# Kernel optimization log

Hardware: AMD Instinct MI355X
Metric: run time of the kernel (lower is better)

The kernel has to match this reference:

```python
import jax, jax.numpy as jnp
import numpy as np

N_HEAD = 16
N_KV_HEAD = 8
HEAD_DIM = 64
EPS_NORM = 1e-6


def _rms_norm(x):
    # F.rms_norm without learned weight
    return x * jax.lax.rsqrt(jnp.mean(x * x, axis=-1, keepdims=True) + EPS_NORM)


def _apply_rotary_emb(x, cos, sin):
    # x: [B, T, H, D]; cos/sin: [T, 1, D/2] (broadcast over B and H)
    d = x.shape[-1] // 2
    x1, x2 = x[..., :d], x[..., d:]
    return jnp.concatenate([x1 * cos + x2 * sin, -x1 * sin + x2 * cos], axis=-1)


def setup_inputs() -> dict:
    key = jax.random.key(0)
    ks = jax.random.split(key, 8)
    B, T, C = 2, 2048, 1024
    return {
        "x": jax.random.normal(ks[0], (B, T, C), jnp.float32),
        "cos": jax.random.uniform(ks[1], (T, 1, HEAD_DIM // 2), jnp.float32),
        "sin": jax.random.uniform(ks[2], (T, 1, HEAD_DIM // 2), jnp.float32),
        "Wq": jax.random.normal(ks[3], (N_HEAD * HEAD_DIM, C), jnp.float32) * 0.02,
        "Wk": jax.random.normal(ks[4], (N_KV_HEAD * HEAD_DIM, C), jnp.float32) * 0.02,
        "Wv": jax.random.normal(ks[5], (N_KV_HEAD * HEAD_DIM, C), jnp.float32) * 0.02,
        "Wproj": jax.random.normal(ks[6], (C, C), jnp.float32) * 0.02,
        "w_braid": jax.random.normal(ks[7], (HEAD_DIM,), jnp.float32),
    }


def reference(x, cos, sin, Wq, Wk, Wv, Wproj, w_braid):
    B, T, C = x.shape
    q = (x @ Wq.T).reshape(B, T, N_HEAD, HEAD_DIM)
    k = (x @ Wk.T).reshape(B, T, N_KV_HEAD, HEAD_DIM)
    v = (x @ Wv.T).reshape(B, T, N_KV_HEAD, HEAD_DIM)
    q = _rms_norm(_apply_rotary_emb(q, cos, sin))
    k = _rms_norm(_apply_rotary_emb(k, cos, sin))
    # [B, H, T, D]
    q = q.transpose(0, 2, 1, 3)
    k = k.transpose(0, 2, 1, 3)
    v = v.transpose(0, 2, 1, 3)
    rep = N_HEAD // N_KV_HEAD
    k = jnp.repeat(k, rep, axis=1)  # GQA repeat_kv_heads
    v = jnp.repeat(v, rep, axis=1)
    # rank-1 outer-sum score: s_q[i] + s_k[j]
    s_q = jnp.einsum("bhtd,d->bht", q, w_braid)
    s_k = jnp.einsum("bhsd,d->bhs", k, w_braid)
    scores = s_q[..., :, None] + s_k[..., None, :]  # [B, H, T, T]
    causal = jnp.arange(T)[:, None] >= jnp.arange(T)[None, :]
    scores = jnp.where(causal, scores, -jnp.inf)
    attn = jax.nn.sigmoid(scores)  # non-softmax gating
    y = jnp.einsum("bhts,bhsd->bhtd", attn, v)
    y = y / (T ** 0.5 + 1e-6)
    y = y.transpose(0, 2, 1, 3).reshape(B, T, C)
    return y @ Wproj.T
```

## Files before the change

kernel.cpp:

```cpp
#include <hip/hip_runtime.h>

#define BATCH   2
#define T_LEN   2048
#define C_DIM   1024
#define NH      16
#define NKV     8
#define HD      64

typedef unsigned short u16;
typedef __attribute__((ext_vector_type(8))) short short8;
typedef __attribute__((ext_vector_type(4))) float floatx4;

__device__ __forceinline__ u16 f2bf(float f) {
    union { float f; unsigned u; } v; v.f = f;
    unsigned r = v.u + 0x7FFF + ((v.u >> 16) & 1);
    return (u16)(r >> 16);
}

__device__ __forceinline__ float bf2f(u16 b) {
    union { unsigned u; float f; } v; v.u = ((unsigned)b) << 16;
    return v.f;
}

__device__ __forceinline__ void gload_lds16(const u16* g, u16* l) {
    __builtin_amdgcn_global_load_lds(
        (const __attribute__((address_space(1))) void*)g,
        (__attribute__((address_space(3))) void*)l, 16, 0, 0);
}

__global__ __launch_bounds__(256)
void cvt_all(const float* __restrict__ x, const float* __restrict__ Wq,
             const float* __restrict__ Wk, const float* __restrict__ Wv,
             const float* __restrict__ Wp, u16* __restrict__ xb,
             u16* __restrict__ Wqkvb, u16* __restrict__ Wpb) {
    const int blk = blockIdx.x;
    const float* src; u16* dst; long off;
    if (blk < 4096)      { src = x;  dst = xb;              off = (long)blk * 1024; }
    else if (blk < 5120) { src = Wq; dst = Wqkvb;           off = (long)(blk - 4096) * 1024; }
    else if (blk < 5632) { src = Wk; dst = Wqkvb + 1048576; off = (long)(blk - 5120) * 1024; }
    else if (blk < 6144) { src = Wv; dst = Wqkvb + 1572864; off = (long)(blk - 5632) * 1024; }
    else                 { src = Wp; dst = Wpb;             off = (long)(blk - 6144) * 1024; }
    const long i = off + (long)threadIdx.x * 4;
    const float4 f = *(const float4*)&src[i];
    ushort4 o;
    o.x = f2bf(f.x); o.y = f2bf(f.y); o.z = f2bf(f.z); o.w = f2bf(f.w);
    *(ushort4*)&dst[i] = o;
}

__global__ __launch_bounds__(256)
void gemm_bf16_nt_b16(const u16* __restrict__ A, const u16* __restrict__ B,
                      u16* __restrict__ C, int M, int N, int K) {
    __shared__ u16 As[128 * 32];
    __shared__ u16 Bs[128 * 32];
    const int tid    = threadIdx.x;
    const int lane   = tid & 63;
    const int wave   = tid >> 6;
    const int row_in = lane & 15;
    const int quad   = lane >> 4;
    const int koff   = quad * 8;
    const int rw     = (wave & 1) * 64;
    const int cw     = (wave >> 1) * 64;
    const int row0   = blockIdx.y * 128;
    const int col0   = blockIdx.x * 128;

    floatx4 acc[4][4] = {};

    for (int k0 = 0; k0 < K; k0 += 32) {
        #pragma unroll
        for (int c = 0; c < 2; ++c) {
            const int l  = c * 256 + tid;
            const int r  = l >> 2;
            const int kc = l & 3;
            gload_lds16(A + (size_t)(row0 + r) * K + k0 + kc * 8, &As[(size_t)l * 8]);
            gload_lds16(B + (size_t)(col0 + r) * K + k0 + kc * 8, &Bs[(size_t)l * 8]);
        }
        __syncthreads();
        short8 af[4], bf_[4];
        #pragma unroll
        for (int i = 0; i < 4; ++i)
            af[i] = *(const short8*)&As[(rw + 16 * i + row_in) * 32 + koff];
        #pragma unroll
        for (int j = 0; j < 4; ++j)
            bf_[j] = *(const short8*)&Bs[(cw + 16 * j + row_in) * 32 + koff];
        #pragma unroll
        for (int i = 0; i < 4; ++i)
            #pragma unroll
            for (int j = 0; j < 4; ++j)
                acc[i][j] = __builtin_amdgcn_mfma_f32_16x16x32_bf16(af[i], bf_[j], acc[i][j], 0, 0, 0);
        __syncthreads();
    }

    #pragma unroll
    for (int i = 0; i < 4; ++i)
        #pragma unroll
        for (int j = 0; j < 4; ++j)
            #pragma unroll
            for (int r = 0; r < 4; ++r)
                C[(size_t)(row0 + rw + 16 * i + quad * 4 + r) * N + col0 + cw + 16 * j + row_in]
                    = f2bf(acc[i][j][r]);
    }

__global__ __launch_bounds__(256)
void gemm_bf16_nt2(const u16* __restrict__ A, const u16* __restrict__ B,
                   float* __restrict__ C, int M, int N, int K) {
    __shared__ u16 As[128 * 32];
    __shared__ u16 Bs[64 * 32];
    const int tid    = threadIdx.x;
    const int lane   = tid & 63;
    const int wave   = tid >> 6;
    const int row_in = lane & 15;
    const int quad   = lane >> 4;
    const int koff   = quad * 8;
    const int rw     = (wave & 1) * 64;
    const int cw     = (wave >> 1) * 32;
    const int row0   = blockIdx.y * 128;
    const int col0   = blockIdx.x * 64;

    floatx4 acc[4][2] = {};

    for (int k0 = 0; k0 < K; k0 += 32) {
        #pragma unroll
        for (int c = 0; c < 2; ++c) {
            const int l  = c * 256 + tid;
            const int r  = l >> 2;
            const int kc = l & 3;
            gload_lds16(A + (size_t)(row0 + r) * K + k0 + kc * 8, &As[(size_t)l * 8]);
        }
        {
            const int r  = tid >> 2;
            const int kc = tid & 3;
            gload_lds16(B + (size_t)(col0 + r) * K + k0 + kc * 8, &Bs[(size_t)tid * 8]);
        }
        __syncthreads();
        short8 af[4], bf_[2];
        #pragma unroll
        for (int i = 0; i < 4; ++i)
            af[i] = *(const short8*)&As[(rw + 16 * i + row_in) * 32 + koff];
        #pragma unroll
        for (int j = 0; j < 2; ++j)
            bf_[j] = *(const short8*)&Bs[(cw + 16 * j + row_in) * 32 + koff];
        #pragma unroll
        for (int i = 0; i < 4; ++i)
            #pragma unroll
            for (int j = 0; j < 2; ++j)
                acc[i][j] = __builtin_amdgcn_mfma_f32_16x16x32_bf16(af[i], bf_[j], acc[i][j], 0, 0, 0);
        __syncthreads();
    }

    #pragma unroll
    for (int i = 0; i < 4; ++i)
        #pragma unroll
        for (int j = 0; j < 2; ++j)
            #pragma unroll
            for (int r = 0; r < 4; ++r)
                C[(size_t)(row0 + rw + 16 * i + quad * 4 + r) * N + col0 + cw + 16 * j + row_in]
                    = acc[i][j][r];
}

__global__ __launch_bounds__(256)
void post_qkv(const u16* __restrict__ qkvb, const float* __restrict__ cosb,
              const float* __restrict__ sinb, const float* __restrict__ wb,
              float* __restrict__ esq, float* __restrict__ esk,
              u16* __restrict__ Vt) {
    __shared__ u16 Lu[64][72];
    const int blk = blockIdx.x;
    const int tid = threadIdx.x;

    if (blk < 512) {
        const int bkv = blk >> 5;
        const int t0  = (blk & 31) * 64;
        const int b   = bkv >> 3;
        const int kvh = bkv & 7;
        const u16* src = qkvb + ((size_t)b * T_LEN + t0) * 2048 + 1536 + kvh * 64;
        #pragma unroll
        for (int c = 0; c < 2; ++c) {
            const int i = c * 256 + tid;
            const int s = i >> 3, d0 = (i & 7) * 8;
            *(short8*)&Lu[s][d0] = *(const short8*)&src[(size_t)s * 2048 + d0];
        }
        __syncthreads();
        u16* dst = Vt + (size_t)bkv * 64 * T_LEN + t0;
        #pragma unroll
        for (int c = 0; c < 2; ++c) {
            const int i = c * 256 + tid;
            const int d = i >> 3, s0 = (i & 7) * 8;
            short8 o;
            #pragma unroll
            for (int j = 0; j < 8; ++j) o[j] = (short)Lu[s0 + j][d];
            *(short8*)&dst[(size_t)d * T_LEN + s0] = o;
        }
        return;
    }

    const int wave = tid >> 6;
    const int lane = tid & 63;
    const long vec = (long)(blk - 512) * 4 + wave;
    const u16* src; float* dst; int t;
    if (vec < 65536) {
        const int h = (int)(vec & 15);
        const long bt = vec >> 4;
        t = (int)(bt & 2047);
        const int b = (int)(bt >> 11);
        src = qkvb + bt * 2048 + h * 64;
        dst = esq + ((long)b * NH + h) * T_LEN + t;
    } else {
        const long vk = vec - 65536;
        const int h = (int)(vk & 7);
        const long bt = vk >> 3;
        t = (int)(bt & 2047);
        const int b = (int)(bt >> 11);
        src = qkvb + bt * 2048 + 1024 + h * 64;
        dst = esk + ((long)b * NKV + h) * T_LEN + t;
    }

    const float v  = bf2f(src[lane]);
    const float ot = __shfl_xor(v, 32, 64);
    const int j = lane & 31;
    const float x1 = (lane < 32) ? v : ot;
    const float x2 = (lane < 32) ? ot : v;
    const float c  = cosb[t * 32 + j];
    const float s  = sinb[t * 32 + j];
    const float r  = (lane < 32) ? fmaf(x1, c, x2 * s) : fmaf(x2, c, -x1 * s);

    float ss = r * r;
    #pragma unroll
    for (int m = 1; m < 64; m <<= 1) ss += __shfl_xor(ss, m, 64);
    const float scale = rsqrtf(ss * (1.0f / 64.0f) + 1e-6f);

    float dt = r * scale * wb[lane];
    #pragma unroll
    for (int m = 1; m < 64; m <<= 1) dt += __shfl_xor(dt, m, 64);
    if (lane == 0)
        *dst = __expf(-fminf(fmaxf(dt, -44.0f), 44.0f));
}

__global__ __launch_bounds__(512)
void braid_attn(const float* __restrict__ esq, const float* __restrict__ esk,
                const u16* __restrict__ Vt, u16* __restrict__ yb) {
    __shared__ u16 Vd[2][4096];
    __shared__ float eskl[128];
    float* red = (float*)&Vd[0][0];

    const int bh   = blockIdx.y;
    const int b    = bh >> 4;
    const int h    = bh & 15;
    const int p    = blockIdx.x;
    const int tid  = threadIdx.x;
    const int lane = tid & 63;
    const int wave = tid >> 6;
    const int sg   = wave >> 2;
    const int w4   = wave & 3;
    const int n    = lane & 15;
    const int quad = lane >> 4;
    const int row  = w4 * 16 + n;

    const float* esq_p = esq + (size_t)bh * T_LEN;
    const float* esk_p = esk + ((size_t)b * NKV + (h >> 1)) * T_LEN;
    const u16*   vt_b  = Vt + ((size_t)b * NKV + (h >> 1)) * 64 * T_LEN;
    const float  inv   = (float)(1.0 / (45.254833995939045 + 1e-6));

    for (int ph = 0; ph < 2; ++ph) {
        const int t0 = (ph ? p : (31 - p)) * 64;
        const float a = esq_p[t0 + row];
        const int send = t0 + 64;
        floatx4 acc[4] = {};

        for (int s0 = 0; s0 < send; s0 += 128) {
            __syncthreads();
            {
                const int r = tid >> 3, g = tid & 7;
                const int so = (g ^ (r & 7)) << 3;
                gload_lds16(vt_b + (size_t)r * T_LEN + s0 + so, &Vd[0][(size_t)tid * 8]);
                if (s0 + 64 < send)
                    gload_lds16(vt_b + (size_t)r * T_LEN + s0 + 64 + so, &Vd[1][(size_t)tid * 8]);
            }
            if (tid < 128 && (tid < 64 || s0 + 64 < send))
                eskl[tid] = esk_p[s0 + tid];
            __syncthreads();

            const int s0g = s0 + sg * 64;
            if (s0g < send) {
                const bool diag = (s0g == t0);
                #pragma unroll
                for (int kk = 0; kk < 2; ++kk) {
                    const float* eb = &eskl[sg * 64 + kk * 32 + quad * 8];
                    const float4 e0 = *(const float4*)eb;
                    const float4 e1 = *(const float4*)(eb + 4);
                    const float ev[8] = {e0.x, e0.y, e0.z, e0.w, e1.x, e1.y, e1.z, e1.w};
                    union { unsigned u[4]; short8 s8; } af;
                    #pragma unroll
                    for (int jj = 0; jj < 4; ++jj) {
                        float r0 = __builtin_amdgcn_rcpf(fmaf(ev[2 * jj],     a, 1.0f));
                        float r1 = __builtin_amdgcn_rcpf(fmaf(ev[2 * jj + 1], a, 1.0f));
                        if (diag) {
                            const int s_ = kk * 32 + quad * 8 + 2 * jj;
                            if (s_     > row) r0 = 0.0f;
                            if (s_ + 1 > row) r1 = 0.0f;
                        }
                        af.u[jj] = __builtin_amdgcn_perm(__float_as_uint(r1),
                                                         __float_as_uint(r0), 0x07060302u);
                    }
                    #pragma unroll
                    for (int j = 0; j < 4; ++j) {
                        const short8 bfr = *(const short8*)
                            &Vd[sg][(16 * j + n) * 64 + (((kk * 4 + quad) ^ (n & 7)) << 3)];
                        acc[j] = __builtin_amdgcn_mfma_f32_16x16x32_bf16(af.s8, bfr, acc[j], 0, 0, 0);
                    }
                }
            }
        }

        __syncthreads();
        if (sg == 1) {
            #pragma unroll
            for (int j = 0; j < 4; ++j)
                #pragma unroll
                for (int r = 0; r < 4; ++r)
                    red[(j * 4 + r) * 256 + w4 * 64 + lane] = acc[j][r];
        }
        __syncthreads();
        if (sg == 0) {
            #pragma unroll
            for (int j = 0; j < 4; ++j)
                #pragma unroll
                for (int r = 0; r < 4; ++r) {
                    const float o = acc[j][r] + red[(j * 4 + r) * 256 + w4 * 64 + lane];
                    const int t = t0 + w4 * 16 + quad * 4 + r;
                    yb[((size_t)b * T_LEN + t) * C_DIM + h * HD + 16 * j + n] = f2bf(o * inv);
                }
        }
    }
}

extern "C" void kernel_launch(void* const* d_in, const int* in_sizes, int n_in,
                              void* d_out, int out_size, void* d_ws, size_t ws_size,
                              hipStream_t stream) {
    const float* x     = (const float*)d_in[0];
    const float* cosb  = (const float*)d_in[1];
    const float* sinb  = (const float*)d_in[2];
    const float* Wq    = (const float*)d_in[3];
    const float* Wk    = (const float*)d_in[4];
    const float* Wv    = (const float*)d_in[5];
    const float* Wproj = (const float*)d_in[6];
    const float* wb    = (const float*)d_in[7];
    float* out = (float*)d_out;

    char* w = (char*)d_ws;
    u16* xb     = (u16*)w;  w += (size_t)4096 * 1024 * 2;
    u16* Wqkvb  = (u16*)w;  w += (size_t)2048 * 1024 * 2;
    u16* Wpb    = (u16*)w;  w += (size_t)1024 * 1024 * 2;
    u16* qkvb   = (u16*)w;  w += (size_t)4096 * 2048 * 2;
    u16* yb     = (u16*)w;  w += (size_t)4096 * 1024 * 2;
    u16* VtB    = (u16*)w;  w += (size_t)BATCH * NKV * 64 * T_LEN * 2;
    float* esq  = (float*)w; w += (size_t)BATCH * NH * T_LEN * 4;
    float* esk  = (float*)w; w += (size_t)BATCH * NKV * T_LEN * 4;

    dim3 blk(256);
    cvt_all<<<7168, blk, 0, stream>>>(x, Wq, Wk, Wv, Wproj, xb, Wqkvb, Wpb);
    gemm_bf16_nt_b16<<<dim3(16, 32), blk, 0, stream>>>(xb, Wqkvb, qkvb, 4096, 2048, 1024);
    post_qkv<<<512 + 24576, blk, 0, stream>>>(qkvb, cosb, sinb, wb, esq, esk, VtB);
    braid_attn<<<dim3(16, 32), dim3(512), 0, stream>>>(esq, esk, VtB, yb);
    gemm_bf16_nt2<<<dim3(16, 32), blk, 0, stream>>>(yb, Wpb, out, 4096, 1024, 1024);
}
```

Measured before the change: 180.2 us.

## Fuse rotary, RMS norm and braid score into QKV GEMM epilogue

```diff
diff --git a/kernel.cpp b/kernel.cpp
--- a/kernel.cpp
+++ b/kernel.cpp
@@ -15,11 +15,6 @@
     union { float f; unsigned u; } v; v.f = f;
     unsigned r = v.u + 0x7FFF + ((v.u >> 16) & 1);
     return (u16)(r >> 16);
-}
-
-__device__ __forceinline__ float bf2f(u16 b) {
-    union { unsigned u; float f; } v; v.u = ((unsigned)b) << 16;
-    return v.f;
 }
 
 __device__ __forceinline__ void gload_lds16(const u16* g, u16* l) {
@@ -48,8 +43,11 @@
 }
 
 __global__ __launch_bounds__(256)
-void gemm_bf16_nt_b16(const u16* __restrict__ A, const u16* __restrict__ B,
-                      u16* __restrict__ C, int M, int N, int K) {
+void gemm_qkv(const u16* __restrict__ A, const u16* __restrict__ B,
+              u16* __restrict__ vb, float* __restrict__ esq,
+              float* __restrict__ esk, const float* __restrict__ cosb,
+              const float* __restrict__ sinb, const float* __restrict__ wb) {
+    const int K = 1024;
     __shared__ u16 As[128 * 32];
     __shared__ u16 Bs[128 * 32];
     const int tid    = threadIdx.x;
@@ -90,148 +88,84 @@
         __syncthreads();
     }
 
-    #pragma unroll
-    for (int i = 0; i < 4; ++i)
-        #pragma unroll
-        for (int j = 0; j < 4; ++j)
-            #pragma unroll
-            for (int r = 0; r < 4; ++r)
-                C[(size_t)(row0 + rw + 16 * i + quad * 4 + r) * N + col0 + cw + 16 * j + row_in]
-                    = f2bf(acc[i][j][r]);
-    }
+    const int n    = row_in;
+    const int cw_g = col0 + cw;
+    const int rw_g = row0 + rw;
+    const int ch   = cw_g >> 6;
+
+    if (ch < 24) {
+        const float w0 = wb[n], w1 = wb[16 + n], w2 = wb[32 + n], w3 = wb[48 + n];
+        #pragma unroll
+        for (int i = 0; i < 4; ++i)
+            #pragma unroll
+            for (int r = 0; r < 4; ++r) {
+                const int grow = rw_g + 16 * i + quad * 4 + r;
+                const int t = grow & 2047;
+                const int b = grow >> 11;
+                const float c0 = cosb[t * 32 + n];
+                const float c1 = cosb[t * 32 + 16 + n];
+                const float s0 = sinb[t * 32 + n];
+                const float s1 = sinb[t * 32 + 16 + n];
+                const float x0 = acc[i][0][r], x1 = acc[i][1][r];
+                const float x2 = acc[i][2][r], x3 = acc[i][3][r];
+                const float r0 = fmaf(x0, c0,  x2 * s0);
+                const float r1 = fmaf(x1, c1,  x3 * s1);
+                const float r2 = fmaf(x2, c0, -x0 * s0);
+                const float r3 = fmaf(x3, c1, -x1 * s1);
+                float ss = r0 * r0 + r1 * r1 + r2 * r2 + r3 * r3;
+                float dt = r0 * w0 + r1 * w1 + r2 * w2 + r3 * w3;
+                #pragma unroll
+                for (int m = 1; m < 16; m <<= 1) {
+                    ss += __shfl_xor(ss, m, 64);
+                    dt += __shfl_xor(dt, m, 64);
+                }
+                const float val = dt * rsqrtf(ss * (1.0f / 64.0f) + 1e-6f);
+                const float e = __expf(-fminf(fmaxf(val, -44.0f), 44.0f));
+                if (n == 0) {
+                    if (ch < 16) esq[((size_t)b * NH + ch) * T_LEN + t] = e;
+                    else         esk[((size_t)b * NKV + ch - 16) * T_LEN + t] = e;
+                }
+            }
+    } else {
+        const int vcol = cw_g - 1536;
+        #pragma unroll
+        for (int i = 0; i < 4; ++i)
+            #pragma unroll
+            for (int j = 0; j < 4; ++j)
+                #pragma unroll
+                for (int r = 0; r < 4; ++r)
+                    vb[(size_t)(rw_g + 16 * i + quad * 4 + r) * 512 + vcol + 16 * j + n]
+                        = f2bf(acc[i][j][r]);
+    }
+}
 
 __global__ __launch_bounds__(256)
-void gemm_bf16_nt2(const u16* __restrict__ A, const u16* __restrict__ B,
-                   float* __restrict__ C, int M, int N, int K) {
-    __shared__ u16 As[128 * 32];
-    __shared__ u16 Bs[64 * 32];
-    const int tid    = threadIdx.x;
-    const int lane   = tid & 63;
-    const int wave   = tid >> 6;
-    const int row_in = lane & 15;
-    const int quad   = lane >> 4;
-    const int koff   = quad * 8;
-    const int rw     = (wave & 1) * 64;
-    const int cw     = (wave >> 1) * 32;
-    const int row0   = blockIdx.y * 128;
-    const int col0   = blockIdx.x * 64;
-
-    floatx4 acc[4][2] = {};
-
-    for (int k0 = 0; k0 < K; k0 += 32) {
-        #pragma unroll
-        for (int c = 0; c < 2; ++c) {
-            const int l  = c * 256 + tid;
-            const int r  = l >> 2;
-            const int kc = l & 3;
-            gload_lds16(A + (size_t)(row0 + r) * K + k0 + kc * 8, &As[(size_t)l * 8]);
-        }
-        {
-            const int r  = tid >> 2;
-            const int kc = tid & 3;
-            gload_lds16(B + (size_t)(col0 + r) * K + k0 + kc * 8, &Bs[(size_t)tid * 8]);
-        }
-        __syncthreads();
-        short8 af[4], bf_[2];
-        #pragma unroll
-        for (int i = 0; i < 4; ++i)
-            af[i] = *(const short8*)&As[(rw + 16 * i + row_in) * 32 + koff];
-        #pragma unroll
-        for (int j = 0; j < 2; ++j)
-            bf_[j] = *(const short8*)&Bs[(cw + 16 * j + row_in) * 32 + koff];
-        #pragma unroll
-        for (int i = 0; i < 4; ++i)
-            #pragma unroll
-            for (int j = 0; j < 2; ++j)
-                acc[i][j] = __builtin_amdgcn_mfma_f32_16x16x32_bf16(af[i], bf_[j], acc[i][j], 0, 0, 0);
-        __syncthreads();
-    }
-
-    #pragma unroll
-    for (int i = 0; i < 4; ++i)
-        #pragma unroll
-        for (int j = 0; j < 2; ++j)
-            #pragma unroll
-            for (int r = 0; r < 4; ++r)
-                C[(size_t)(row0 + rw + 16 * i + quad * 4 + r) * N + col0 + cw + 16 * j + row_in]
-                    = acc[i][j][r];
-}
-
-__global__ __launch_bounds__(256)
-void post_qkv(const u16* __restrict__ qkvb, const float* __restrict__ cosb,
-              const float* __restrict__ sinb, const float* __restrict__ wb,
-              float* __restrict__ esq, float* __restrict__ esk,
-              u16* __restrict__ Vt) {
+void vt_convert(const u16* __restrict__ vb, u16* __restrict__ Vt) {
     __shared__ u16 Lu[64][72];
     const int blk = blockIdx.x;
     const int tid = threadIdx.x;
-
-    if (blk < 512) {
-        const int bkv = blk >> 5;
-        const int t0  = (blk & 31) * 64;
-        const int b   = bkv >> 3;
-        const int kvh = bkv & 7;
-        const u16* src = qkvb + ((size_t)b * T_LEN + t0) * 2048 + 1536 + kvh * 64;
-        #pragma unroll
-        for (int c = 0; c < 2; ++c) {
-            const int i = c * 256 + tid;
-            const int s = i >> 3, d0 = (i & 7) * 8;
-            *(short8*)&Lu[s][d0] = *(const short8*)&src[(size_t)s * 2048 + d0];
-        }
-        __syncthreads();
-        u16* dst = Vt + (size_t)bkv * 64 * T_LEN + t0;
-        #pragma unroll
-        for (int c = 0; c < 2; ++c) {
-            const int i = c * 256 + tid;
-            const int d = i >> 3, s0 = (i & 7) * 8;
-            short8 o;
-            #pragma unroll
-            for (int j = 0; j < 8; ++j) o[j] = (short)Lu[s0 + j][d];
-            *(short8*)&dst[(size_t)d * T_LEN + s0] = o;
-        }
-        return;
-    }
-
-    const int wave = tid >> 6;
-    const int lane = tid & 63;
-    const long vec = (long)(blk - 512) * 4 + wave;
-    const u16* src; float* dst; int t;
-    if (vec < 65536) {
-        const int h = (int)(vec & 15);
-        const long bt = vec >> 4;
-        t = (int)(bt & 2047);
-        const int b = (int)(bt >> 11);
-        src = qkvb + bt * 2048 + h * 64;
-        dst = esq + ((long)b * NH + h) * T_LEN + t;
-    } else {
-        const long vk = vec - 65536;
-        const int h = (int)(vk & 7);
-        const long bt = vk >> 3;
-        t = (int)(bt & 2047);
-        const int b = (int)(bt >> 11);
-        src = qkvb + bt * 2048 + 1024 + h * 64;
-        dst = esk + ((long)b * NKV + h) * T_LEN + t;
-    }
-
-    const float v  = bf2f(src[lane]);
-    const float ot = __shfl_xor(v, 32, 64);
-    const int j = lane & 31;
-    const float x1 = (lane < 32) ? v : ot;
-    const float x2 = (lane < 32) ? ot : v;
-    const float c  = cosb[t * 32 + j];
-    const float s  = sinb[t * 32 + j];
-    const float r  = (lane < 32) ? fmaf(x1, c, x2 * s) : fmaf(x2, c, -x1 * s);
-
-    float ss = r * r;
+    const int bkv = blk >> 5;
+    const int t0  = (blk & 31) * 64;
+    const int b   = bkv >> 3;
+    const int kvh = bkv & 7;
+    const u16* src = vb + ((size_t)b * T_LEN + t0) * 512 + kvh * 64;
     #pragma unroll
-    for (int m = 1; m < 64; m <<= 1) ss += __shfl_xor(ss, m, 64);
-    const float scale = rsqrtf(ss * (1.0f / 64.0f) + 1e-6f);
-
-    float dt = r * scale * wb[lane];
+    for (int c = 0; c < 2; ++c) {
+        const int i = c * 256 + tid;
+        const int s = i >> 3, d0 = (i & 7) * 8;
+        *(short8*)&Lu[s][d0] = *(const short8*)&src[(size_t)s * 512 + d0];
+    }
+    __syncthreads();
+    u16* dst = Vt + (size_t)bkv * 64 * T_LEN + t0;
     #pragma unroll
-    for (int m = 1; m < 64; m <<= 1) dt += __shfl_xor(dt, m, 64);
-    if (lane == 0)
-        *dst = __expf(-fminf(fmaxf(dt, -44.0f), 44.0f));
+    for (int c = 0; c < 2; ++c) {
+        const int i = c * 256 + tid;
+        const int d = i >> 3, s0 = (i & 7) * 8;
+        short8 o;
+        #pragma unroll
+        for (int j = 0; j < 8; ++j) o[j] = (short)Lu[s0 + j][d];
+        *(short8*)&dst[(size_t)d * T_LEN + s0] = o;
+    }
 }
 
 __global__ __launch_bounds__(512)
@@ -332,6 +266,63 @@
     }
 }
 
+__global__ __launch_bounds__(256)
+void gemm_bf16_nt2(const u16* __restrict__ A, const u16* __restrict__ B,
+                   float* __restrict__ C, int M, int N, int K) {
+    __shared__ u16 As[128 * 32];
+    __shared__ u16 Bs[64 * 32];
+    const int tid    = threadIdx.x;
+    const int lane   = tid & 63;
+    const int wave   = tid >> 6;
+    const int row_in = lane & 15;
+    const int quad   = lane >> 4;
+    const int koff   = quad * 8;
+    const int rw     = (wave & 1) * 64;
+    const int cw     = (wave >> 1) * 32;
+    const int row0   = blockIdx.y * 128;
+    const int col0   = blockIdx.x * 64;
+
+    floatx4 acc[4][2] = {};
+
+    for (int k0 = 0; k0 < K; k0 += 32) {
+        #pragma unroll
+        for (int c = 0; c < 2; ++c) {
+            const int l  = c * 256 + tid;
+            const int r  = l >> 2;
+            const int kc = l & 3;
+            gload_lds16(A + (size_t)(row0 + r) * K + k0 + kc * 8, &As[(size_t)l * 8]);
+        }
+        {
+            const int r  = tid >> 2;
+            const int kc = tid & 3;
+            gload_lds16(B + (size_t)(col0 + r) * K + k0 + kc * 8, &Bs[(size_t)tid * 8]);
+        }
+        __syncthreads();
+        short8 af[4], bf_[2];
+        #pragma unroll
+        for (int i = 0; i < 4; ++i)
+            af[i] = *(const short8*)&As[(rw + 16 * i + row_in) * 32 + koff];
+        #pragma unroll
+        for (int j = 0; j < 2; ++j)
+            bf_[j] = *(const short8*)&Bs[(cw + 16 * j + row_in) * 32 + koff];
+        #pragma unroll
+        for (int i = 0; i < 4; ++i)
+            #pragma unroll
+            for (int j = 0; j < 2; ++j)
+                acc[i][j] = __builtin_amdgcn_mfma_f32_16x16x32_bf16(af[i], bf_[j], acc[i][j], 0, 0, 0);
+        __syncthreads();
+    }
+
+    #pragma unroll
+    for (int i = 0; i < 4; ++i)
+        #pragma unroll
+        for (int j = 0; j < 2; ++j)
+            #pragma unroll
+            for (int r = 0; r < 4; ++r)
+                C[(size_t)(row0 + rw + 16 * i + quad * 4 + r) * N + col0 + cw + 16 * j + row_in]
+                    = acc[i][j][r];
+}
+
 extern "C" void kernel_launch(void* const* d_in, const int* in_sizes, int n_in,
                               void* d_out, int out_size, void* d_ws, size_t ws_size,
                               hipStream_t stream) {
@@ -349,7 +340,7 @@
     u16* xb     = (u16*)w;  w += (size_t)4096 * 1024 * 2;
     u16* Wqkvb  = (u16*)w;  w += (size_t)2048 * 1024 * 2;
     u16* Wpb    = (u16*)w;  w += (size_t)1024 * 1024 * 2;
-    u16* qkvb   = (u16*)w;  w += (size_t)4096 * 2048 * 2;
+    u16* vb     = (u16*)w;  w += (size_t)4096 * 512 * 2;
     u16* yb     = (u16*)w;  w += (size_t)4096 * 1024 * 2;
     u16* VtB    = (u16*)w;  w += (size_t)BATCH * NKV * 64 * T_LEN * 2;
     float* esq  = (float*)w; w += (size_t)BATCH * NH * T_LEN * 4;
@@ -357,8 +348,8 @@
 
     dim3 blk(256);
     cvt_all<<<7168, blk, 0, stream>>>(x, Wq, Wk, Wv, Wproj, xb, Wqkvb, Wpb);
-    gemm_bf16_nt_b16<<<dim3(16, 32), blk, 0, stream>>>(xb, Wqkvb, qkvb, 4096, 2048, 1024);
-    post_qkv<<<512 + 24576, blk, 0, stream>>>(qkvb, cosb, sinb, wb, esq, esk, VtB);
+    gemm_qkv<<<dim3(16, 32), blk, 0, stream>>>(xb, Wqkvb, vb, esq, esk, cosb, sinb, wb);
+    vt_convert<<<512, blk, 0, stream>>>(vb, VtB);
     braid_attn<<<dim3(16, 32), dim3(512), 0, stream>>>(esq, esk, VtB, yb);
     gemm_bf16_nt2<<<dim3(16, 32), blk, 0, stream>>>(yb, Wpb, out, 4096, 1024, 1024);
 }
```

After: 168.1 us. -6.7%, faster.
